# Kernel tuning notes

Hardware: AMD Instinct MI355X
Metric: run time of the kernel (lower is better)

Reference implementation:

```python
import jax, jax.numpy as jnp
import numpy as np

B, T, D = 32, 512, 1024
HOP, HID = 8, 350
NEG = jnp.float32(-1e30)  # stand-in for -inf in masked softmax (grad-safe)


def setup_inputs() -> dict:
    key = jax.random.key(0)
    ks = jax.random.split(key, 8)
    s = lambda k, sh, sc: (jax.random.normal(k, sh, jnp.float32) * sc)
    return {
        "input": jax.random.normal(ks[0], (B, T, D), jnp.float32),
        "lg": T,  # unused by the module's forward, kept for signature fidelity
        "W0": s(ks[1], (D, 3 * D), 0.02),
        "b0": jnp.zeros((2 * D,), jnp.float32),
        "W1": s(ks[2], (D, 3 * D), 0.02),
        "b1": jnp.zeros((2 * D,), jnp.float32),
        "ws1": s(ks[3], (HID, D), 0.02),
        "ws2": s(ks[4], (HOP, HID), 0.02),
        "fc_w": s(ks[5], (D, HOP * D), 0.02),
        "fc_b": jnp.zeros((D,), jnp.float32),
    }


def sru_layer(x, W, b):
    # x: [T, B, d]; SRU with use_tanh=True, identity highway (d_in == d_out).
    d = W.shape[1] // 3
    U = jnp.einsum('tbi,ij->tbj', x, W)            # one big GEMM for all gates
    xt = U[..., :d]
    f = jax.nn.sigmoid(U[..., d:2 * d] + b[:d])    # forget gate
    r = jax.nn.sigmoid(U[..., 2 * d:] + b[d:])     # reset/highway gate

    def step(c, u):
        xt_t, f_t = u
        c = f_t * c + (1.0 - f_t) * xt_t
        return c, c

    c0 = jnp.zeros(xt.shape[1:], xt.dtype)
    _, cs = jax.lax.scan(step, c0, (xt, f))        # elementwise gated recurrence
    return r * jnp.tanh(cs) + (1.0 - r) * x


def reference(input, lg, W0, b0, W1, b1, ws1, ws2, fc_w, fc_b):
    # lengths per _process_lengths: T - count of positions where feature-0 == 0
    lengths = T - jnp.sum((input[:, :, 0] == 0).astype(jnp.int32), axis=1)  # [B]

    x = jnp.transpose(input, (1, 0, 2))            # [T, B, D]
    x = sru_layer(x, W0, b0)
    x = sru_layer(x, W1, b1)
    x = jnp.transpose(x, (1, 0, 2))                # [B, T, D]

    # multi-hop self-attention pooling (dropout is identity in eval mode)
    hbar = jnp.tanh(jnp.einsum('btd,hd->bth', x, ws1))   # [B, T, HID]
    alphas = jnp.einsum('bth,kh->bkt', hbar, ws2)        # [B, HOP, T]
    mask = jnp.arange(T)[None, None, :] >= lengths[:, None, None]
    attn = jax.nn.softmax(jnp.where(mask, NEG, alphas), axis=2)  # [B, HOP, T]

    pooled = jnp.einsum('bkt,btd->bkd', attn, x).reshape(input.shape[0], -1)
    out = pooled @ fc_w.T + fc_b                   # [B, D]
    return out, attn
```

## Files before the change

### kernel.cpp

```cpp
#include <hip/hip_runtime.h>
#include <hip/hip_bf16.h>

#define B_ 32
#define T_ 512
#define D_ 1024
#define HOP_ 8
#define HID_ 350
#define NEGV -1e30f
#define CH_ 4

typedef __bf16 v8bf __attribute__((ext_vector_type(8)));
typedef float  v4f  __attribute__((ext_vector_type(4)));

__device__ __forceinline__ float fast_sigmoid(float x) {
    return 1.0f / (1.0f + __expf(-x));
}
__device__ __forceinline__ float fast_tanh(float x) {
    return 1.0f - 2.0f / (__expf(2.0f * x) + 1.0f);
}
__device__ __forceinline__ float bf2f(unsigned short u) {
    unsigned x = ((unsigned)u) << 16;
    float f;
    __builtin_memcpy(&f, &x, 4);
    return f;
}
__device__ __forceinline__ unsigned short f2bf(float v) {
    __hip_bfloat16 h = __float2bfloat16(v);
    unsigned short u;
    __builtin_memcpy(&u, &h, 2);
    return u;
}

__global__ __launch_bounds__(512) void lengths_k(const float* __restrict__ input,
                                                 int* __restrict__ len) {
    int b = blockIdx.x;
    int t = threadIdx.x;
    int z = (input[((size_t)b * T_ + t) * D_] == 0.0f) ? 1 : 0;
    __shared__ int cnt;
    if (t == 0) cnt = 0;
    __syncthreads();
    unsigned long long m = __ballot(z);
    if ((t & 63) == 0) atomicAdd(&cnt, __popcll(m));
    __syncthreads();
    if (t == 0) len[b] = T_ - cnt;
}


__global__ __launch_bounds__(256) void convX_k(const float* __restrict__ in,
                                               unsigned short* __restrict__ out) {
    int i = (blockIdx.x * 256 + threadIdx.x) * 4;
    float4 v = *(const float4*)&in[i];
    out[i + 0] = f2bf(v.x);
    out[i + 1] = f2bf(v.y);
    out[i + 2] = f2bf(v.z);
    out[i + 3] = f2bf(v.w);
}

template <bool NT>
__global__ __launch_bounds__(256) void convW_k(const float* __restrict__ W,
                                               unsigned short* __restrict__ Wp,
                                               int K, int N, int nT, int Nreal) {
    int o = blockIdx.x * 256 + threadIdx.x;
    int tile = o >> 12;
    int within = o & 4095;
    int n_l = within >> 5, k_l = within & 31;
    int kb = tile / nT, nbb = tile % nT;
    int n = nbb * 128 + n_l, k = kb * 32 + k_l;
    float v = 0.f;
    if (NT) {
        if (n < Nreal) v = W[(size_t)n * K + k];
    } else {
        v = W[(size_t)k * N + n];
    }
    Wp[o] = f2bf(v);
}

template <int EPI>
__global__ __launch_bounds__(256) void gemm_mfma(
    const unsigned short* __restrict__ A,
    const unsigned short* __restrict__ Bp,
    void* __restrict__ C,
    int K, int nT, int Nstore) {
    __shared__ __align__(16) char smem[34816];
    unsigned short* As = (unsigned short*)smem;
    unsigned short* Bs = (unsigned short*)(smem + 8192);
    const int tid = threadIdx.x;
    const int lane = tid & 63;
    const int wid = __builtin_amdgcn_readfirstlane(tid >> 6);
    const int wm = wid & 1, wn = wid >> 1;
    const int m0 = blockIdx.y * 128;
    const int n0 = blockIdx.x * 128;
    const int nb = blockIdx.x;
    const int quad = lane >> 4;
    const int l15 = lane & 15;

    v4f acc[4][4];
#pragma unroll
    for (int i = 0; i < 4; ++i)
#pragma unroll
        for (int j = 0; j < 4; ++j) acc[i][j] = (v4f)(0.f);

    const int nKB = K >> 5;
    for (int kb = 0; kb < nKB; ++kb) {
        __syncthreads();
#pragma unroll
        for (int p = 0; p < 2; ++p) {
            int g = p * 256 + wid * 64 + lane;
            const unsigned short* gp = A + (size_t)(m0 + (g >> 2)) * K + kb * 32 + (g & 3) * 8;
            int ldsOff = (p * 256 + wid * 64) * 16;
            __builtin_amdgcn_global_load_lds(
                (const __attribute__((address_space(1))) void*)gp,
                (__attribute__((address_space(3))) void*)((char*)As + ldsOff),
                16, 0, 0);
        }
        const unsigned short* bt = Bp + (size_t)(kb * nT + nb) * (128 * 32);
#pragma unroll
        for (int p = 0; p < 2; ++p) {
            int g = p * 256 + wid * 64 + lane;
            const unsigned short* gp = bt + g * 8;
            int ldsOff = (p * 256 + wid * 64) * 16;
            __builtin_amdgcn_global_load_lds(
                (const __attribute__((address_space(1))) void*)gp,
                (__attribute__((address_space(3))) void*)((char*)Bs + ldsOff),
                16, 0, 0);
        }
        __syncthreads();
        v8bf af[4], bfr[4];
#pragma unroll
        for (int mi = 0; mi < 4; ++mi)
            af[mi] = *(const v8bf*)&As[(wm * 64 + mi * 16 + l15) * 32 + quad * 8];
#pragma unroll
        for (int ni = 0; ni < 4; ++ni)
            bfr[ni] = *(const v8bf*)&Bs[(wn * 64 + ni * 16 + l15) * 32 + quad * 8];
#pragma unroll
        for (int mi = 0; mi < 4; ++mi)
#pragma unroll
            for (int ni = 0; ni < 4; ++ni)
                acc[mi][ni] = __builtin_amdgcn_mfma_f32_16x16x32_bf16(
                    af[mi], bfr[ni], acc[mi][ni], 0, 0, 0);
    }

    if (EPI == 0) {
        __syncthreads();
        unsigned short* Ct = (unsigned short*)smem;
#pragma unroll
        for (int ni = 0; ni < 4; ++ni) {
            int n_l = wn * 64 + ni * 16 + l15;
#pragma unroll
            for (int mi = 0; mi < 4; ++mi) {
                int m_l = wm * 64 + mi * 16 + quad * 4;
                v4f cc = acc[mi][ni];
#pragma unroll
                for (int r = 0; r < 4; ++r)
                    Ct[(m_l + r) * 136 + n_l] = f2bf(cc[r]);
            }
        }
        __syncthreads();
        int row = tid >> 1;
        int colH = (tid & 1) << 6;
        unsigned short* gdst = (unsigned short*)C + (size_t)(m0 + row) * 3072 + n0 + colH;
        const unsigned short* lsrc = Ct + row * 136 + colH;
#pragma unroll
        for (int i = 0; i < 8; ++i) {
            uint4 v = *(const uint4*)(lsrc + i * 8);
            *(uint4*)(gdst + i * 8) = v;
        }
    } else {
        const int baseM = m0 + wm * 64;
        const int baseN = n0 + wn * 64;
        float* Cf = (float*)C;
#pragma unroll
        for (int ni = 0; ni < 4; ++ni) {
            int j = baseN + ni * 16 + l15;
            if (j < Nstore) {
#pragma unroll
                for (int mi = 0; mi < 4; ++mi) {
                    int m = baseM + mi * 16 + quad * 4;
                    v4f c = acc[mi][ni];
#pragma unroll
                    for (int r = 0; r < 4; ++r)
                        Cf[(size_t)(m + r) * Nstore + j] = fast_tanh(c[r]);
                }
            }
        }
    }
}

__global__ __launch_bounds__(512) void sru_scan_seg(
    const unsigned short* __restrict__ Up,
    const float* __restrict__ bias,
    const unsigned short* __restrict__ xres,
    unsigned short* __restrict__ xout) {
    int b = blockIdx.x >> 4;
    int d0 = (blockIdx.x & 15) << 6;
    int dl = threadIdx.x & 63;
    int s = threadIdx.x >> 6;
    int d = d0 + dl;
    float bf = bias[d], br = bias[D_ + d];
    const unsigned short* Ub = Up + (size_t)b * T_ * 3072 + d;
    const int t0 = s * 64;

    float Aa = 1.f, Bv = 0.f;
    for (int tt = 0; tt < 64; tt += 8) {
        float xt[8], fv[8];
#pragma unroll
        for (int j = 0; j < 8; ++j) {
            const unsigned short* u = Ub + (size_t)(t0 + tt + j) * 3072;
            xt[j] = bf2f(u[0]);
            fv[j] = bf2f(u[1024]);
        }
#pragma unroll
        for (int j = 0; j < 8; ++j) {
            float f = fast_sigmoid(fv[j] + bf);
            Aa *= f;
            Bv = f * Bv + (1.f - f) * xt[j];
        }
    }
    __shared__ float Asm[8][64], Bsm[8][64], cinS[8][64];
    Asm[s][dl] = Aa;
    Bsm[s][dl] = Bv;
    __syncthreads();
    if (threadIdx.x < 64) {
        float c = 0.f;
#pragma unroll
        for (int ss = 0; ss < 8; ++ss) {
            cinS[ss][threadIdx.x] = c;
            c = Asm[ss][threadIdx.x] * c + Bsm[ss][threadIdx.x];
        }
    }
    __syncthreads();
    float c = cinS[s][dl];
    const unsigned short* xr = xres + (size_t)b * T_ * D_ + d;
    unsigned short* ob = xout + (size_t)b * T_ * D_ + d;
    for (int tt = 0; tt < 64; tt += 4) {
        float xt[4], fv[4], rv[4], xv[4];
#pragma unroll
        for (int j = 0; j < 4; ++j) {
            const unsigned short* u = Ub + (size_t)(t0 + tt + j) * 3072;
            xt[j] = bf2f(u[0]);
            fv[j] = bf2f(u[1024]);
            rv[j] = bf2f(u[2048]);
            xv[j] = bf2f(xr[(size_t)(t0 + tt + j) * D_]);
        }
#pragma unroll
        for (int j = 0; j < 4; ++j) {
            float f = fast_sigmoid(fv[j] + bf);
            float r = fast_sigmoid(rv[j] + br);
            c = f * c + (1.f - f) * xt[j];
            float o = r * fast_tanh(c) + (1.f - r) * xv[j];
            ob[(size_t)(t0 + tt + j) * D_] = f2bf(o);
        }
    }
}


template <bool BT, bool DO_TANH>
__global__ __launch_bounds__(256) void gemm64(const float* __restrict__ A,
                                              const float* __restrict__ Bm,
                                              float* __restrict__ C,
                                              int M, int N, int K) {
    __shared__ float Asm[16][64];
    __shared__ float Bsm[16][64];
    const int tid = threadIdx.x;
    const int tx = tid & 15;
    const int ty = tid >> 4;
    const int m0 = blockIdx.y * 64;
    const int n0 = blockIdx.x * 64;
    float acc[4][4] = {};
    const int ar = tid >> 2;
    const int ac = (tid & 3) << 2;

    for (int k0 = 0; k0 < K; k0 += 16) {
        {
            float4 v = *(const float4*)&A[(size_t)(m0 + ar) * K + k0 + ac];
            Asm[ac + 0][ar] = v.x; Asm[ac + 1][ar] = v.y;
            Asm[ac + 2][ar] = v.z; Asm[ac + 3][ar] = v.w;
        }
        if (!BT) {
            int kk = tid >> 4;
            int c4 = (tid & 15) << 2;
            float4 v = *(const float4*)&Bm[(size_t)(k0 + kk) * N + n0 + c4];
            Bsm[kk][c4 + 0] = v.x; Bsm[kk][c4 + 1] = v.y;
            Bsm[kk][c4 + 2] = v.z; Bsm[kk][c4 + 3] = v.w;
        } else {
            int nn = tid >> 2;
            int kk = (tid & 3) << 2;
            int row = n0 + nn;
            if (row < N) {
                float4 v = *(const float4*)&Bm[(size_t)row * K + k0 + kk];
                Bsm[kk + 0][nn] = v.x; Bsm[kk + 1][nn] = v.y;
                Bsm[kk + 2][nn] = v.z; Bsm[kk + 3][nn] = v.w;
            } else {
                Bsm[kk + 0][nn] = 0.f; Bsm[kk + 1][nn] = 0.f;
                Bsm[kk + 2][nn] = 0.f; Bsm[kk + 3][nn] = 0.f;
            }
        }
        __syncthreads();
#pragma unroll
        for (int kk = 0; kk < 16; ++kk) {
            float4 a = *(const float4*)&Asm[kk][ty << 2];
            float4 b = *(const float4*)&Bsm[kk][tx << 2];
            float am[4] = {a.x, a.y, a.z, a.w};
            float bm[4] = {b.x, b.y, b.z, b.w};
#pragma unroll
            for (int i = 0; i < 4; ++i)
#pragma unroll
                for (int j = 0; j < 4; ++j)
                    acc[i][j] += am[i] * bm[j];
        }
        __syncthreads();
    }
#pragma unroll
    for (int i = 0; i < 4; ++i) {
        int row = m0 + (ty << 2) + i;
#pragma unroll
        for (int j = 0; j < 4; ++j) {
            int col = n0 + (tx << 2) + j;
            if (col < N) {
                float v = acc[i][j];
                if (DO_TANH) v = fast_tanh(v);
                C[(size_t)row * N + col] = v;
            }
        }
    }
}

__global__ __launch_bounds__(256) void sru_scan(const float* __restrict__ U,
                                                const float* __restrict__ bias,
                                                const float* __restrict__ xin,
                                                float* __restrict__ xout) {
    int idx = blockIdx.x * 256 + threadIdx.x;
    int b = idx >> 10;
    int d = idx & (D_ - 1);
    float bfv = bias[d], br = bias[D_ + d];
    float c = 0.0f;
    const float* Ub = U + (size_t)b * T_ * (3 * D_);
    const float* xb = xin + (size_t)b * T_ * D_;
    float* ob = xout + (size_t)b * T_ * D_;
    for (int t = 0; t < T_; t += 8) {
        float ux[8], uf[8], ur[8], xv[8];
#pragma unroll
        for (int j = 0; j < 8; ++j) {
            const float* u = Ub + (size_t)(t + j) * (3 * D_);
            ux[j] = u[d];
            uf[j] = u[D_ + d];
            ur[j] = u[2 * D_ + d];
            xv[j] = xb[(size_t)(t + j) * D_ + d];
        }
#pragma unroll
        for (int j = 0; j < 8; ++j) {
            float f = fast_sigmoid(uf[j] + bfv);
            float r = fast_sigmoid(ur[j] + br);
            c = f * c + (1.0f - f) * ux[j];
            ob[(size_t)(t + j) * D_ + d] = r * fast_tanh(c) + (1.0f - r) * xv[j];
        }
    }
}


__global__ __launch_bounds__(256) void alphas_k(const float* __restrict__ hbar,
                                                const float* __restrict__ ws2,
                                                float* __restrict__ alph) {
    __shared__ float w[HOP_][352];
    for (int i = threadIdx.x; i < HOP_ * HID_; i += 256)
        w[i / HID_][i % HID_] = ws2[i];
    __syncthreads();
    int bt = blockIdx.x * 256 + threadIdx.x;
    const float* hr = hbar + (size_t)bt * HID_;
    float acc[HOP_] = {};
    for (int h = 0; h < HID_; ++h) {
        float hv = hr[h];
#pragma unroll
        for (int k = 0; k < HOP_; ++k) acc[k] += w[k][h] * hv;
    }
    float* ar = alph + (size_t)bt * HOP_;
#pragma unroll
    for (int k = 0; k < HOP_; ++k) ar[k] = acc[k];
}

__global__ __launch_bounds__(256) void softmax_k(const float* __restrict__ alph,
                                                 const int* __restrict__ len,
                                                 float* __restrict__ attn) {
    int b = blockIdx.x >> 3, k = blockIdx.x & 7;
    int L = len[b];
    int t0 = threadIdx.x, t1 = threadIdx.x + 256;
    float v0 = (t0 >= L) ? NEGV : alph[((size_t)b * T_ + t0) * HOP_ + k];
    float v1 = (t1 >= L) ? NEGV : alph[((size_t)b * T_ + t1) * HOP_ + k];
    __shared__ float redm[4];
    __shared__ float reds[4];
    float m = fmaxf(v0, v1);
#pragma unroll
    for (int off = 32; off; off >>= 1) m = fmaxf(m, __shfl_xor(m, off));
    if ((threadIdx.x & 63) == 0) redm[threadIdx.x >> 6] = m;
    __syncthreads();
    m = fmaxf(fmaxf(redm[0], redm[1]), fmaxf(redm[2], redm[3]));
    float e0 = __expf(v0 - m), e1 = __expf(v1 - m);
    float s = e0 + e1;
#pragma unroll
    for (int off = 32; off; off >>= 1) s += __shfl_xor(s, off);
    if ((threadIdx.x & 63) == 0) reds[threadIdx.x >> 6] = s;
    __syncthreads();
    s = reds[0] + reds[1] + reds[2] + reds[3];
    float inv = 1.0f / s;
    float* ar = attn + ((size_t)b * HOP_ + k) * T_;
    ar[t0] = e0 * inv;
    ar[t1] = e1 * inv;
}

__global__ __launch_bounds__(256) void pooled_bf_k(const float* __restrict__ attn,
                                                   const unsigned short* __restrict__ x2b,
                                                   float* __restrict__ pooled) {
    __shared__ float at[HOP_][T_];
    int b = blockIdx.x >> 2;
    int d0 = (blockIdx.x & 3) * 256;
    for (int i = threadIdx.x; i < HOP_ * T_; i += 256)
        at[i >> 9][i & (T_ - 1)] = attn[(size_t)b * HOP_ * T_ + i];
    __syncthreads();
    int d = d0 + threadIdx.x;
    float acc[HOP_] = {};
    const unsigned short* xb = x2b + (size_t)b * T_ * D_ + d;
    for (int t = 0; t < T_; ++t) {
        float xv = bf2f(xb[(size_t)t * D_]);
#pragma unroll
        for (int k = 0; k < HOP_; ++k) acc[k] += at[k][t] * xv;
    }
#pragma unroll
    for (int k = 0; k < HOP_; ++k)
        pooled[((size_t)b * HOP_ + k) * D_ + d] = acc[k];
}

__global__ __launch_bounds__(256) void pooled_k(const float* __restrict__ attn,
                                                const float* __restrict__ x2,
                                                float* __restrict__ pooled) {
    __shared__ float at[HOP_][T_];
    int b = blockIdx.x >> 2;
    int d0 = (blockIdx.x & 3) * 256;
    for (int i = threadIdx.x; i < HOP_ * T_; i += 256)
        at[i >> 9][i & (T_ - 1)] = attn[(size_t)b * HOP_ * T_ + i];
    __syncthreads();
    int d = d0 + threadIdx.x;
    float acc[HOP_] = {};
    const float* xb = x2 + (size_t)b * T_ * D_ + d;
    for (int t = 0; t < T_; ++t) {
        float xv = xb[(size_t)t * D_];
#pragma unroll
        for (int k = 0; k < HOP_; ++k) acc[k] += at[k][t] * xv;
    }
#pragma unroll
    for (int k = 0; k < HOP_; ++k)
        pooled[((size_t)b * HOP_ + k) * D_ + d] = acc[k];
}

__global__ __launch_bounds__(256) void fc_k(const float* __restrict__ pooled,
                                            const float* __restrict__ fcw,
                                            const float* __restrict__ fcb,
                                            float* __restrict__ out) {
    __shared__ float w[8][1028];
    int j0 = blockIdx.x * 8;
    int b = threadIdx.x >> 3, jj = threadIdx.x & 7;
    float acc = 0.0f;
    for (int p0 = 0; p0 < HOP_ * D_; p0 += 1024) {
        __syncthreads();
        for (int i = threadIdx.x * 4; i < 8 * 1024; i += 256 * 4) {
            int r = i >> 10, c = i & 1023;
            *(float4*)&w[r][c] = *(const float4*)&fcw[(size_t)(j0 + r) * (HOP_ * D_) + p0 + c];
        }
        __syncthreads();
        const float* pr = pooled + (size_t)b * (HOP_ * D_) + p0;
#pragma unroll 4
        for (int i = 0; i < 1024; i += 4) {
            float4 wv = *(const float4*)&w[jj][i];
            float4 pv = *(const float4*)&pr[i];
            acc += wv.x * pv.x + wv.y * pv.y + wv.z * pv.z + wv.w * pv.w;
        }
    }
    out[(size_t)b * D_ + j0 + jj] = acc + fcb[j0 + jj];
}

extern "C" void kernel_launch(void* const* d_in, const int* in_sizes, int n_in,
                              void* d_out, int out_size, void* d_ws, size_t ws_size,
                              hipStream_t stream) {
    const float* input = (const float*)d_in[0];
    const float* W0   = (const float*)d_in[2];
    const float* b0   = (const float*)d_in[3];
    const float* W1   = (const float*)d_in[4];
    const float* b1   = (const float*)d_in[5];
    const float* ws1  = (const float*)d_in[6];
    const float* ws2  = (const float*)d_in[7];
    const float* fc_w = (const float*)d_in[8];
    const float* fc_b = (const float*)d_in[9];

    float* out  = (float*)d_out;
    float* attn = out + (size_t)B_ * D_;
    (void)in_sizes; (void)n_in; (void)out_size;

    const int M = B_ * T_;
    char* ws = (char*)d_ws;

    const size_t NEED_A = 181141632ull;
    const size_t NEED_B = 80478336ull;
    const size_t NEED_FB = 100663424ull;

    if (ws_size >= NEED_B) {
        const int CHv = (ws_size >= NEED_A) ? 32 : 8;
        const size_t szU = (size_t)CHv * 512 * 3072 * 2;
        const size_t szX = (size_t)CHv * 512 * 1024 * 2;
        unsigned short* Uc   = (unsigned short*)ws;
        unsigned short* xbc  = (unsigned short*)(ws + szU);
        unsigned short* x2b  = (unsigned short*)(ws + szU + szX);
        unsigned short* W0p  = (unsigned short*)(ws + szU + szX + 33554432);
        unsigned short* W1p  = W0p + 3145728;
        unsigned short* ws1p = W1p + 3145728;
        int*            len  = (int*)(ws1p + 393216);
        float* hbar   = (float*)ws;
        float* alph   = (float*)(ws + 22937600);
        float* pooled = (float*)(ws + 23461888);

        lengths_k<<<B_, 512, 0, stream>>>(input, len);
        convW_k<false><<<(D_ * 3 * D_) / 256, 256, 0, stream>>>(W0, W0p, D_, 3 * D_, 24, 3 * D_);
        convW_k<false><<<(D_ * 3 * D_) / 256, 256, 0, stream>>>(W1, W1p, D_, 3 * D_, 24, 3 * D_);
        convW_k<true><<<(D_ * 384) / 256, 256, 0, stream>>>(ws1, ws1p, D_, 384, 3, HID_);

        for (int c0 = 0; c0 < B_; c0 += CHv) {
            const float* inC = input + (size_t)c0 * T_ * D_;
            const int Mc = CHv * T_;
            convX_k<<<(Mc * D_ / 4) / 256, 256, 0, stream>>>(inC, xbc);
            gemm_mfma<0><<<dim3(24, Mc / 128), 256, 0, stream>>>(xbc, W0p, Uc, D_, 24, 0);
            sru_scan_seg<<<CHv * 16, 512, 0, stream>>>(Uc, b0, xbc, xbc);
            gemm_mfma<0><<<dim3(24, Mc / 128), 256, 0, stream>>>(xbc, W1p, Uc, D_, 24, 0);
            sru_scan_seg<<<CHv * 16, 512, 0, stream>>>(
                Uc, b1, xbc, x2b + (size_t)c0 * T_ * D_);
        }

        gemm_mfma<1><<<dim3(3, M / 128), 256, 0, stream>>>(x2b, ws1p, hbar, D_, 3, HID_);

        alphas_k<<<M / 256, 256, 0, stream>>>(hbar, ws2, alph);
        softmax_k<<<B_ * HOP_, 256, 0, stream>>>(alph, len, attn);
        pooled_bf_k<<<B_ * 4, 256, 0, stream>>>(attn, x2b, pooled);
        fc_k<<<D_ / 8, 256, 0, stream>>>(pooled, fc_w, fc_b, out);
        return;
    }

    if (ws_size < NEED_FB) return;

    float* U    = (float*)ws;
    float* x1c  = (float*)(ws + 25165824);
    float* x2   = (float*)(ws + 33554432);
    int*   len  = (int*)(ws + 100663296);
    float* hbar   = (float*)ws;
    float* alph   = (float*)(ws + 22937600);
    float* pooled = (float*)(ws + 23461888);

    lengths_k<<<B_, 512, 0, stream>>>(input, len);

    const int Mc = CH_ * T_;
    for (int c0 = 0; c0 < B_; c0 += CH_) {
        const float* inC = input + (size_t)c0 * T_ * D_;
        float* x2C = x2 + (size_t)c0 * T_ * D_;
        gemm64<false, false><<<dim3(3 * D_ / 64, Mc / 64), 256, 0, stream>>>(
            inC, W0, U, Mc, 3 * D_, D_);
        sru_scan<<<CH_ * D_ / 256, 256, 0, stream>>>(U, b0, inC, x1c);
        gemm64<false, false><<<dim3(3 * D_ / 64, Mc / 64), 256, 0, stream>>>(
            x1c, W1, U, Mc, 3 * D_, D_);
        sru_scan<<<CH_ * D_ / 256, 256, 0, stream>>>(U, b1, x1c, x2C);
    }

    gemm64<true, true><<<dim3((HID_ + 63) / 64, M / 64), 256, 0, stream>>>(
        x2, ws1, hbar, M, HID_, D_);
    alphas_k<<<M / 256, 256, 0, stream>>>(hbar, ws2, alph);
    softmax_k<<<B_ * HOP_, 256, 0, stream>>>(alph, len, attn);
    pooled_k<<<B_ * 4, 256, 0, stream>>>(attn, x2, pooled);
    fc_k<<<D_ / 8, 256, 0, stream>>>(pooled, fc_w, fc_b, out);
}
```

Baseline: 781.6 us.

## Store SRU gate projections transposed so the scan reads time-contiguous vectors

The gate GEMM epilogue now writes U transposed ([3D][M]) through shared memory, so each gate channel's time series is contiguous. The SRU scan then loads 8 consecutive timesteps per gate with one 16-byte vector load, where it previously issued strided 2-byte loads per timestep. This targets the uncoalesced gather in the recurrence. In exchange the GEMM's shared-memory transpose pattern changes, which may add bank conflicts, and the residual x reads stay strided.

```diff
diff --git a/kernel.cpp b/kernel.cpp
--- a/kernel.cpp
+++ b/kernel.cpp
@@ -80,7 +80,7 @@
     const unsigned short* __restrict__ A,
     const unsigned short* __restrict__ Bp,
     void* __restrict__ C,
-    int K, int nT, int Nstore) {
+    int K, int nT, int ldc) {
     __shared__ __align__(16) char smem[34816];
     unsigned short* As = (unsigned short*)smem;
     unsigned short* Bs = (unsigned short*)(smem + 8192);
@@ -150,15 +150,16 @@
             for (int mi = 0; mi < 4; ++mi) {
                 int m_l = wm * 64 + mi * 16 + quad * 4;
                 v4f cc = acc[mi][ni];
-#pragma unroll
-                for (int r = 0; r < 4; ++r)
-                    Ct[(m_l + r) * 136 + n_l] = f2bf(cc[r]);
+                ushort4 pk;
+                pk.x = f2bf(cc[0]); pk.y = f2bf(cc[1]);
+                pk.z = f2bf(cc[2]); pk.w = f2bf(cc[3]);
+                *(ushort4*)&Ct[n_l * 136 + m_l] = pk;
             }
         }
         __syncthreads();
         int row = tid >> 1;
         int colH = (tid & 1) << 6;
-        unsigned short* gdst = (unsigned short*)C + (size_t)(m0 + row) * 3072 + n0 + colH;
+        unsigned short* gdst = (unsigned short*)C + (size_t)(n0 + row) * ldc + m0 + colH;
         const unsigned short* lsrc = Ct + row * 136 + colH;
 #pragma unroll
         for (int i = 0; i < 8; ++i) {
@@ -172,14 +173,14 @@
 #pragma unroll
         for (int ni = 0; ni < 4; ++ni) {
             int j = baseN + ni * 16 + l15;
-            if (j < Nstore) {
+            if (j < ldc) {
 #pragma unroll
                 for (int mi = 0; mi < 4; ++mi) {
                     int m = baseM + mi * 16 + quad * 4;
                     v4f c = acc[mi][ni];
 #pragma unroll
                     for (int r = 0; r < 4; ++r)
-                        Cf[(size_t)(m + r) * Nstore + j] = fast_tanh(c[r]);
+                        Cf[(size_t)(m + r) * ldc + j] = fast_tanh(c[r]);
                 }
             }
         }
@@ -187,33 +188,32 @@
 }
 
 __global__ __launch_bounds__(512) void sru_scan_seg(
-    const unsigned short* __restrict__ Up,
+    const unsigned short* __restrict__ Ut,
     const float* __restrict__ bias,
     const unsigned short* __restrict__ xres,
-    unsigned short* __restrict__ xout) {
+    unsigned short* __restrict__ xout,
+    int Mtot) {
     int b = blockIdx.x >> 4;
     int d0 = (blockIdx.x & 15) << 6;
     int dl = threadIdx.x & 63;
     int s = threadIdx.x >> 6;
     int d = d0 + dl;
     float bf = bias[d], br = bias[D_ + d];
-    const unsigned short* Ub = Up + (size_t)b * T_ * 3072 + d;
+    size_t mb = (size_t)b * T_;
+    const unsigned short* xtp = Ut + (size_t)d * Mtot + mb;
+    const unsigned short* ffp = Ut + (size_t)(D_ + d) * Mtot + mb;
+    const unsigned short* rrp = Ut + (size_t)(2 * D_ + d) * Mtot + mb;
     const int t0 = s * 64;
 
     float Aa = 1.f, Bv = 0.f;
     for (int tt = 0; tt < 64; tt += 8) {
-        float xt[8], fv[8];
+        v8bf xtv = *(const v8bf*)&xtp[t0 + tt];
+        v8bf fvv = *(const v8bf*)&ffp[t0 + tt];
 #pragma unroll
         for (int j = 0; j < 8; ++j) {
-            const unsigned short* u = Ub + (size_t)(t0 + tt + j) * 3072;
-            xt[j] = bf2f(u[0]);
-            fv[j] = bf2f(u[1024]);
-        }
-#pragma unroll
-        for (int j = 0; j < 8; ++j) {
-            float f = fast_sigmoid(fv[j] + bf);
+            float f = fast_sigmoid((float)fvv[j] + bf);
             Aa *= f;
-            Bv = f * Bv + (1.f - f) * xt[j];
+            Bv = f * Bv + (1.f - f) * (float)xtv[j];
         }
     }
     __shared__ float Asm[8][64], Bsm[8][64], cinS[8][64];
@@ -230,23 +230,21 @@
     }
     __syncthreads();
     float c = cinS[s][dl];
-    const unsigned short* xr = xres + (size_t)b * T_ * D_ + d;
-    unsigned short* ob = xout + (size_t)b * T_ * D_ + d;
-    for (int tt = 0; tt < 64; tt += 4) {
-        float xt[4], fv[4], rv[4], xv[4];
-#pragma unroll
-        for (int j = 0; j < 4; ++j) {
-            const unsigned short* u = Ub + (size_t)(t0 + tt + j) * 3072;
-            xt[j] = bf2f(u[0]);
-            fv[j] = bf2f(u[1024]);
-            rv[j] = bf2f(u[2048]);
+    const unsigned short* xr = xres + mb * D_ + d;
+    unsigned short* ob = xout + mb * D_ + d;
+    for (int tt = 0; tt < 64; tt += 8) {
+        v8bf xtv = *(const v8bf*)&xtp[t0 + tt];
+        v8bf fvv = *(const v8bf*)&ffp[t0 + tt];
+        v8bf rvv = *(const v8bf*)&rrp[t0 + tt];
+        float xv[8];
+#pragma unroll
+        for (int j = 0; j < 8; ++j)
             xv[j] = bf2f(xr[(size_t)(t0 + tt + j) * D_]);
-        }
-#pragma unroll
-        for (int j = 0; j < 4; ++j) {
-            float f = fast_sigmoid(fv[j] + bf);
-            float r = fast_sigmoid(rv[j] + br);
-            c = f * c + (1.f - f) * xt[j];
+#pragma unroll
+        for (int j = 0; j < 8; ++j) {
+            float f = fast_sigmoid((float)fvv[j] + bf);
+            float r = fast_sigmoid((float)rvv[j] + br);
+            c = f * c + (1.f - f) * (float)xtv[j];
             float o = r * fast_tanh(c) + (1.f - r) * xv[j];
             ob[(size_t)(t0 + tt + j) * D_] = f2bf(o);
         }
@@ -503,6 +501,7 @@
 
     if (ws_size >= NEED_B) {
         const int CHv = (ws_size >= NEED_A) ? 32 : 8;
+        const int Mc = CHv * T_;
         const size_t szU = (size_t)CHv * 512 * 3072 * 2;
         const size_t szX = (size_t)CHv * 512 * 1024 * 2;
         unsigned short* Uc   = (unsigned short*)ws;
@@ -523,13 +522,12 @@
 
         for (int c0 = 0; c0 < B_; c0 += CHv) {
             const float* inC = input + (size_t)c0 * T_ * D_;
-            const int Mc = CHv * T_;
             convX_k<<<(Mc * D_ / 4) / 256, 256, 0, stream>>>(inC, xbc);
-            gemm_mfma<0><<<dim3(24, Mc / 128), 256, 0, stream>>>(xbc, W0p, Uc, D_, 24, 0);
-            sru_scan_seg<<<CHv * 16, 512, 0, stream>>>(Uc, b0, xbc, xbc);
-            gemm_mfma<0><<<dim3(24, Mc / 128), 256, 0, stream>>>(xbc, W1p, Uc, D_, 24, 0);
+            gemm_mfma<0><<<dim3(24, Mc / 128), 256, 0, stream>>>(xbc, W0p, Uc, D_, 24, Mc);
+            sru_scan_seg<<<CHv * 16, 512, 0, stream>>>(Uc, b0, xbc, xbc, Mc);
+            gemm_mfma<0><<<dim3(24, Mc / 128), 256, 0, stream>>>(xbc, W1p, Uc, D_, 24, Mc);
             sru_scan_seg<<<CHv * 16, 512, 0, stream>>>(
-                Uc, b1, xbc, x2b + (size_t)c0 * T_ * D_);
+                Uc, b1, xbc, x2b + (size_t)c0 * T_ * D_, Mc);
         }
 
         gemm_mfma<1><<<dim3(3, M / 128), 256, 0, stream>>>(x2b, ws1p, hbar, D_, 3, HID_);
```

Result: slower. 1.038 ms (+32.8%).

## Split SRU scan into 16 time segments of 32 and cache gate values

Applied to the files above, without the earlier changes.

The chunked SRU scan kernel now gives each block 32 feature columns and 16 time segments of 32 steps instead of 64 columns and 8 segments of 64 steps, doubling the grid. In the first pass each thread keeps the loaded x values and computed forget gates in registers, so the second pass no longer reloads them or recomputes the sigmoid. This shortens each thread's serial chain and cuts global reads and sigmoid work. In exchange, each row is read as 64-byte segments rather than 128-byte ones, register pressure rises from the 64 cached floats, and the cross-segment combine step becomes longer.

```diff
diff --git a/kernel.cpp b/kernel.cpp
--- a/kernel.cpp
+++ b/kernel.cpp
@@ -191,39 +191,34 @@
     const float* __restrict__ bias,
     const unsigned short* __restrict__ xres,
     unsigned short* __restrict__ xout) {
-    int b = blockIdx.x >> 4;
-    int d0 = (blockIdx.x & 15) << 6;
-    int dl = threadIdx.x & 63;
-    int s = threadIdx.x >> 6;
+    int b = blockIdx.x >> 5;
+    int d0 = (blockIdx.x & 31) << 5;
+    int dl = threadIdx.x & 31;
+    int s = threadIdx.x >> 5;
     int d = d0 + dl;
     float bf = bias[d], br = bias[D_ + d];
     const unsigned short* Ub = Up + (size_t)b * T_ * 3072 + d;
-    const int t0 = s * 64;
-
+    const int t0 = s * 32;
+
+    float xt[32], fv[32];
     float Aa = 1.f, Bv = 0.f;
-    for (int tt = 0; tt < 64; tt += 8) {
-        float xt[8], fv[8];
-#pragma unroll
-        for (int j = 0; j < 8; ++j) {
-            const unsigned short* u = Ub + (size_t)(t0 + tt + j) * 3072;
-            xt[j] = bf2f(u[0]);
-            fv[j] = bf2f(u[1024]);
-        }
-#pragma unroll
-        for (int j = 0; j < 8; ++j) {
-            float f = fast_sigmoid(fv[j] + bf);
-            Aa *= f;
-            Bv = f * Bv + (1.f - f) * xt[j];
-        }
-    }
-    __shared__ float Asm[8][64], Bsm[8][64], cinS[8][64];
+#pragma unroll
+    for (int j = 0; j < 32; ++j) {
+        const unsigned short* u = Ub + (size_t)(t0 + j) * 3072;
+        xt[j] = bf2f(u[0]);
+        float f = fast_sigmoid(bf2f(u[1024]) + bf);
+        fv[j] = f;
+        Aa *= f;
+        Bv = f * Bv + (1.f - f) * xt[j];
+    }
+    __shared__ float Asm[16][32], Bsm[16][32], cinS[16][32];
     Asm[s][dl] = Aa;
     Bsm[s][dl] = Bv;
     __syncthreads();
-    if (threadIdx.x < 64) {
+    if (threadIdx.x < 32) {
         float c = 0.f;
 #pragma unroll
-        for (int ss = 0; ss < 8; ++ss) {
+        for (int ss = 0; ss < 16; ++ss) {
             cinS[ss][threadIdx.x] = c;
             c = Asm[ss][threadIdx.x] * c + Bsm[ss][threadIdx.x];
         }
@@ -232,24 +227,14 @@
     float c = cinS[s][dl];
     const unsigned short* xr = xres + (size_t)b * T_ * D_ + d;
     unsigned short* ob = xout + (size_t)b * T_ * D_ + d;
-    for (int tt = 0; tt < 64; tt += 4) {
-        float xt[4], fv[4], rv[4], xv[4];
-#pragma unroll
-        for (int j = 0; j < 4; ++j) {
-            const unsigned short* u = Ub + (size_t)(t0 + tt + j) * 3072;
-            xt[j] = bf2f(u[0]);
-            fv[j] = bf2f(u[1024]);
-            rv[j] = bf2f(u[2048]);
-            xv[j] = bf2f(xr[(size_t)(t0 + tt + j) * D_]);
-        }
-#pragma unroll
-        for (int j = 0; j < 4; ++j) {
-            float f = fast_sigmoid(fv[j] + bf);
-            float r = fast_sigmoid(rv[j] + br);
-            c = f * c + (1.f - f) * xt[j];
-            float o = r * fast_tanh(c) + (1.f - r) * xv[j];
-            ob[(size_t)(t0 + tt + j) * D_] = f2bf(o);
-        }
+#pragma unroll
+    for (int j = 0; j < 32; ++j) {
+        int t = t0 + j;
+        float r = fast_sigmoid(bf2f(Ub[(size_t)t * 3072 + 2048]) + br);
+        c = fv[j] * c + (1.f - fv[j]) * xt[j];
+        float xv = bf2f(xr[(size_t)t * D_]);
+        float o = r * fast_tanh(c) + (1.f - r) * xv;
+        ob[(size_t)t * D_] = f2bf(o);
     }
 }
 
@@ -503,6 +488,7 @@
 
     if (ws_size >= NEED_B) {
         const int CHv = (ws_size >= NEED_A) ? 32 : 8;
+        const int Mc = CHv * T_;
         const size_t szU = (size_t)CHv * 512 * 3072 * 2;
         const size_t szX = (size_t)CHv * 512 * 1024 * 2;
         unsigned short* Uc   = (unsigned short*)ws;
@@ -523,12 +509,11 @@
 
         for (int c0 = 0; c0 < B_; c0 += CHv) {
             const float* inC = input + (size_t)c0 * T_ * D_;
-            const int Mc = CHv * T_;
             convX_k<<<(Mc * D_ / 4) / 256, 256, 0, stream>>>(inC, xbc);
             gemm_mfma<0><<<dim3(24, Mc / 128), 256, 0, stream>>>(xbc, W0p, Uc, D_, 24, 0);
-            sru_scan_seg<<<CHv * 16, 512, 0, stream>>>(Uc, b0, xbc, xbc);
+            sru_scan_seg<<<CHv * 32, 512, 0, stream>>>(Uc, b0, xbc, xbc);
             gemm_mfma<0><<<dim3(24, Mc / 128), 256, 0, stream>>>(xbc, W1p, Uc, D_, 24, 0);
-            sru_scan_seg<<<CHv * 16, 512, 0, stream>>>(
+            sru_scan_seg<<<CHv * 32, 512, 0, stream>>>(
                 Uc, b1, xbc, x2b + (size_t)c0 * T_ * D_);
         }
 
```

Measured after the change: 828.8 us. 1.06x slower.
